# Kernel tuning notes

Measured on AMD Instinct MI355X. Metric: run time of the kernel, lower is better.

Reference implementation:

```python
import jax, jax.numpy as jnp
import numpy as np

T, B, F, H, N = 256, 256, 128, 1024, 2


def setup_inputs() -> dict:
    key = jax.random.key(0)
    ks = jax.random.split(key, 12)
    s_in = 1.0 / np.sqrt(H)  # PyTorch LSTM/Linear init scale ~ U(-1/sqrt(H), 1/sqrt(H))
    u = lambda k, shape: jax.random.uniform(k, shape, jnp.float32, -s_in, s_in)
    inp = {
        "x": jax.random.normal(ks[0], (T, B, F), jnp.float32),
        "W_ih0": u(ks[1], (4 * H, F)),
        "W_hh0": u(ks[2], (4 * H, H)),
        "b_ih0": u(ks[3], (4 * H,)),
        "b_hh0": u(ks[4], (4 * H,)),
        "W_ih1": u(ks[5], (4 * H, H)),
        "W_hh1": u(ks[6], (4 * H, H)),
        "b_ih1": u(ks[7], (4 * H,)),
        "b_hh1": u(ks[8], (4 * H,)),
        "W_lin": u(ks[9], (F, H)),
        "b_lin": u(ks[10], (F,)),
        "bs": B,
    }
    return inp


def _lstm_layer(x, W_ih, W_hh, b_ih, b_hh):
    # x: (T, B, in), returns out (T, B, H), (h_T, c_T) each (B, H)
    # Precompute input projections for all timesteps in one big GEMM.
    xW = jnp.einsum('tbf,gf->tbg', x, W_ih) + b_ih + b_hh  # (T, B, 4H)
    h0 = jnp.zeros((x.shape[1], W_hh.shape[1]), x.dtype)

    def step(carry, xw_t):
        h, c = carry
        gates = xw_t + h @ W_hh.T  # (B, 4H); PyTorch gate order i, f, g, o
        i, f, g, o = jnp.split(gates, 4, axis=-1)
        c = jax.nn.sigmoid(f) * c + jax.nn.sigmoid(i) * jnp.tanh(g)
        h = jax.nn.sigmoid(o) * jnp.tanh(c)
        return (h, c), h

    (h_T, c_T), out = jax.lax.scan(step, (h0, h0), xW)
    return out, h_T, c_T


def reference(x, W_ih0, W_hh0, b_ih0, b_hh0, W_ih1, W_hh1, b_ih1, b_hh1, W_lin, b_lin, bs):
    # Stacked 2-layer LSTM with zero initial state (self.h is None on fresh call).
    out0, h0_T, c0_T = _lstm_layer(x, W_ih0, W_hh0, b_ih0, b_hh0)
    out1, h1_T, c1_T = _lstm_layer(out0, W_ih1, W_hh1, b_ih1, b_hh1)
    # Original: y = linear(out[0]) -> first timestep of top layer output.
    y = out1[0] @ W_lin.T + b_lin  # (B, F)
    h_n = jnp.stack([h0_T, h1_T])  # (N, B, H)
    c_n = jnp.stack([c0_T, c1_T])  # (N, B, H)
    return y, h_n, c_n
```

## Files before the change

### kernel.cpp

```cpp
#include <hip/hip_runtime.h>
#include <stdint.h>


typedef __bf16 bf16x8 __attribute__((ext_vector_type(8)));
typedef float  f32x4  __attribute__((ext_vector_type(4)));
typedef unsigned short ushort8v __attribute__((ext_vector_type(8)));
typedef unsigned short ushort4v __attribute__((ext_vector_type(4)));
typedef unsigned short ushort2v __attribute__((ext_vector_type(2)));
typedef __attribute__((address_space(1))) unsigned int as1_u32;
typedef __attribute__((address_space(3))) unsigned int as3_u32;

#define T_STEPS 256
#define BATCH   256
#define HDIM    1024
#define GDIM    4096
#define FDIM    128
#define HXSLOT  (BATCH * HDIM)

static __device__ __forceinline__ float bf2f(unsigned short u) {
  union { unsigned int i; float f; } v; v.i = ((unsigned int)u) << 16; return v.f;
}
static __device__ __forceinline__ unsigned short f2bf(float f) {
  return __builtin_bit_cast(unsigned short, (__bf16)f);
}
static __device__ __forceinline__ float sigm(float x) { return 1.f / (1.f + __expf(-x)); }
static __device__ __forceinline__ float tanh_f(float x) { return 2.f / (1.f + __expf(-2.f * x)) - 1.f; }

static __device__ __forceinline__ int swz(int b) {
  return b ^ (((b >> 7) & 3) << 4);
}
static __device__ __forceinline__ int gswz(int b) {
  return b ^ (((b >> 7) & 7) << 4);
}

static __device__ __forceinline__ void vl1_inv() {
  asm volatile("buffer_inv" ::: "memory");
}

__global__ void conv_bf16(const float* __restrict__ s, unsigned short* __restrict__ d, int n) {
  int i = blockIdx.x * 256 + threadIdx.x;
  if (i < n) d[i] = f2bf(s[i]);
}

__global__ void diag_kernel(float* out, int n, float v) {
  int i = blockIdx.x * 256 + threadIdx.x;
  if (i < n) out[i] = v;
}

__device__ __forceinline__ void post_stamp(unsigned int* st, unsigned int gen, bool fast) {
  if (!fast) __builtin_amdgcn_fence(__ATOMIC_RELEASE, "agent");
  __hip_atomic_store(st, gen, __ATOMIC_RELAXED, __HIP_MEMORY_SCOPE_AGENT);
}

__device__ __forceinline__ void poll_all(unsigned int* stamps, unsigned int target) {
  unsigned int* p = stamps + (threadIdx.x & 31) * 32;
  for (unsigned int it = 0; it < (1u << 15); ++it) {
    unsigned int gv = __hip_atomic_load(p, __ATOMIC_RELAXED, __HIP_MEMORY_SCOPE_AGENT);
    if (__all((int)(gv - target) >= 0)) return;
    if (it > 16) __builtin_amdgcn_s_sleep(1);
  }
}

__device__ __forceinline__ void poll_mine(unsigned int* stamps, int g, int kh, unsigned int target) {
  unsigned int* p = stamps + (kh * 16 + g + 4 * ((int)threadIdx.x & 3)) * 32;
  for (unsigned int it = 0; it < (1u << 15); ++it) {
    unsigned int gv = __hip_atomic_load(p, __ATOMIC_RELAXED, __HIP_MEMORY_SCOPE_AGENT);
    if (__all((int)(gv - target) >= 0)) return;
    if (it > 64) __builtin_amdgcn_s_sleep(1);
  }
}

__device__ __forceinline__ void lds_spin(unsigned int* f, unsigned int need) {
  for (unsigned int it = 0; it < (1u << 15); ++it) {
    unsigned int v = __hip_atomic_load(f, __ATOMIC_ACQUIRE, __HIP_MEMORY_SCOPE_WORKGROUP);
    if ((int)(v - need) >= 0) return;
    if (it > 32) __builtin_amdgcn_s_sleep(1);
  }
}

__device__ __forceinline__ void stage_chunks(const unsigned short* __restrict__ hsrc,
                                             unsigned short* AsPtr, int r0, int g, int kh, int lane) {
  #pragma unroll
  for (int q = 0; q < 4; ++q) {
    int c = kh * 16 + g + 4 * q;
    const char* src = (const char*)(hsrc + (size_t)c * 8192 + r0 * 32);
    char* dst = (char*)AsPtr + c * 2048;
    __builtin_amdgcn_global_load_lds((const as1_u32*)(src + lane * 16), (as3_u32*)dst, 16, 0, 0);
    __builtin_amdgcn_global_load_lds((const as1_u32*)(src + 1024 + lane * 16), (as3_u32*)(dst + 1024), 16, 0, 0);
  }
}

__global__ __launch_bounds__(512, 2) void gemm_bt_xw(
    const unsigned short* __restrict__ A,
    const unsigned short* __restrict__ B,
    unsigned short* __restrict__ xw)
{
  const int tid = threadIdx.x, lane = tid & 63, wv = tid >> 6;
  const int wm = wv & 1, wn = wv >> 1;
  const int quad = lane >> 4, l15 = lane & 15;
  const int m0 = blockIdx.x * 256;
  const int n0 = blockIdx.y * 256;

  __shared__ unsigned short Ab[2][16384];
  __shared__ unsigned short Bb[2][16384];

  f32x4 acc[8][4];
  #pragma unroll
  for (int i = 0; i < 8; ++i)
    #pragma unroll
    for (int j = 0; j < 4; ++j) acc[i][j] = f32x4{0.f, 0.f, 0.f, 0.f};

  #define G2L(dst8k, src, row_org, blk_row0, kt_)                                   \
    {                                                                               \
      int o_ = wv * 1024 + lane * 16;                                               \
      int tp_ = gswz(o_);                                                           \
      int row_ = (blk_row0) + (tp_ >> 7);                                           \
      const char* g_ = (const char*)((src) + (size_t)((row_org) + row_) * 1024)     \
                       + (kt_) * 128 + (tp_ & 127);                                 \
      __builtin_amdgcn_global_load_lds((const as1_u32*)g_,                          \
          (as3_u32*)((char*)(dst8k) + wv * 1024), 16, 0, 0);                        \
    }

  #pragma unroll
  for (int b4 = 0; b4 < 4; ++b4) G2L(&Bb[0][b4 * 4096], B, n0, b4 * 64, 0);
  #pragma unroll
  for (int q4 = 0; q4 < 4; ++q4) G2L(&Ab[0][q4 * 4096], A, m0, q4 * 64, 0);
  __syncthreads();

  bf16x8 af[4][2], bfr[4][2];

  #pragma unroll 1
  for (int kt = 0; kt < 16; ++kt) {
    const int cur = kt & 1, nxt = cur ^ 1;
    const bool st = (kt < 15);

    if (st) { G2L(&Bb[nxt][0], B, n0, 0, kt + 1); G2L(&Bb[nxt][4096], B, n0, 64, kt + 1); }
    if (kt == 15)      asm volatile("s_waitcnt vmcnt(2)" ::: "memory");
    else if (kt > 0)   asm volatile("s_waitcnt vmcnt(4)" ::: "memory");
    __builtin_amdgcn_s_barrier();
    __builtin_amdgcn_sched_barrier(0);
    #pragma unroll
    for (int nt = 0; nt < 4; ++nt)
      #pragma unroll
      for (int kk = 0; kk < 2; ++kk) {
        int q = (wn * 64 + nt * 16 + l15) * 128 + kk * 64 + quad * 16;
        bfr[nt][kk] = *(const bf16x8*)((const char*)Bb[cur] + gswz(q));
      }
    #pragma unroll
    for (int mt = 0; mt < 4; ++mt)
      #pragma unroll
      for (int kk = 0; kk < 2; ++kk) {
        int q = (wm * 128 + mt * 16 + l15) * 128 + kk * 64 + quad * 16;
        af[mt][kk] = *(const bf16x8*)((const char*)Ab[cur] + gswz(q));
      }
    __builtin_amdgcn_s_setprio(1);
    #pragma unroll
    for (int mt = 0; mt < 4; ++mt)
      #pragma unroll
      for (int nt = 0; nt < 2; ++nt)
        #pragma unroll
        for (int kk = 0; kk < 2; ++kk)
          acc[mt][nt] = __builtin_amdgcn_mfma_f32_16x16x32_bf16(af[mt][kk], bfr[nt][kk], acc[mt][nt], 0, 0, 0);
    __builtin_amdgcn_s_setprio(0);
    __builtin_amdgcn_s_barrier();

    if (st) { G2L(&Bb[nxt][8192], B, n0, 128, kt + 1); G2L(&Bb[nxt][12288], B, n0, 192, kt + 1); }
    __builtin_amdgcn_s_barrier();
    __builtin_amdgcn_s_setprio(1);
    #pragma unroll
    for (int mt = 0; mt < 4; ++mt)
      #pragma unroll
      for (int nt = 0; nt < 2; ++nt)
        #pragma unroll
        for (int kk = 0; kk < 2; ++kk)
          acc[mt][nt + 2] = __builtin_amdgcn_mfma_f32_16x16x32_bf16(af[mt][kk], bfr[nt + 2][kk], acc[mt][nt + 2], 0, 0, 0);
    __builtin_amdgcn_s_setprio(0);
    __builtin_amdgcn_s_barrier();

    if (st) { G2L(&Ab[nxt][0], A, m0, 0, kt + 1); G2L(&Ab[nxt][8192], A, m0, 128, kt + 1); }
    if (kt == 15) asm volatile("s_waitcnt vmcnt(0)" ::: "memory");
    else          asm volatile("s_waitcnt vmcnt(6)" ::: "memory");
    __builtin_amdgcn_s_barrier();
    __builtin_amdgcn_sched_barrier(0);
    #pragma unroll
    for (int mt = 0; mt < 4; ++mt)
      #pragma unroll
      for (int kk = 0; kk < 2; ++kk) {
        int q = (wm * 128 + 64 + mt * 16 + l15) * 128 + kk * 64 + quad * 16;
        af[mt][kk] = *(const bf16x8*)((const char*)Ab[cur] + gswz(q));
      }
    __builtin_amdgcn_s_setprio(1);
    #pragma unroll
    for (int mt = 0; mt < 4; ++mt)
      #pragma unroll
      for (int nt = 0; nt < 2; ++nt)
        #pragma unroll
        for (int kk = 0; kk < 2; ++kk)
          acc[mt + 4][nt] = __builtin_amdgcn_mfma_f32_16x16x32_bf16(af[mt][kk], bfr[nt][kk], acc[mt + 4][nt], 0, 0, 0);
    __builtin_amdgcn_s_setprio(0);
    __builtin_amdgcn_s_barrier();

    if (st) { G2L(&Ab[nxt][4096], A, m0, 64, kt + 1); G2L(&Ab[nxt][12288], A, m0, 192, kt + 1); }
    __builtin_amdgcn_s_barrier();
    __builtin_amdgcn_s_setprio(1);
    #pragma unroll
    for (int mt = 0; mt < 4; ++mt)
      #pragma unroll
      for (int nt = 0; nt < 2; ++nt)
        #pragma unroll
        for (int kk = 0; kk < 2; ++kk)
          acc[mt + 4][nt + 2] = __builtin_amdgcn_mfma_f32_16x16x32_bf16(af[mt][kk], bfr[nt + 2][kk], acc[mt + 4][nt + 2], 0, 0, 0);
    __builtin_amdgcn_s_setprio(0);
    __builtin_amdgcn_s_barrier();
  }
  #undef G2L

  #pragma unroll
  for (int mt = 0; mt < 8; ++mt) {
    int ml = wm * 128 + mt * 16 + quad * 4;
    #pragma unroll
    for (int nt = 0; nt < 4; ++nt) {
      int col = n0 + wn * 64 + nt * 16 + l15;
      ushort4v v;
      v.x = f2bf(acc[mt][nt][0]); v.y = f2bf(acc[mt][nt][1]);
      v.z = f2bf(acc[mt][nt][2]); v.w = f2bf(acc[mt][nt][3]);
      *(ushort4v*)(xw + ((size_t)blockIdx.x * GDIM + col) * BATCH + ml) = v;
    }
  }
}

__device__ __forceinline__ bool probe_chk(unsigned int* probeBuf, unsigned int* stamps,
                                          unsigned int salt, unsigned int target,
                                          unsigned int* flagLds) {
  const int wg = blockIdx.x, mi = wg & 7, ni = wg >> 3;
  const int tid = threadIdx.x;
  if (tid == 0) probeBuf[wg * 32] = salt ^ (unsigned int)wg;
  __syncthreads();
  if (tid == 0)
    __hip_atomic_store(stamps + ni * 32, target, __ATOMIC_RELAXED, __HIP_MEMORY_SCOPE_AGENT);
  poll_all(stamps, target);
  vl1_inv();
  if (tid == 0) {
    unsigned int bad = 0;
    for (int k = 0; k < 32; ++k) {
      int member = mi + 8 * k;
      unsigned int v = probeBuf[member * 32];
      if (v != (salt ^ (unsigned int)member)) bad = 1;
    }
    *flagLds = bad;
  }
  __syncthreads();
  return (*flagLds == 0);
}

__global__ __launch_bounds__(512, 2) void lstm_layer0_kernel(
    const unsigned short* __restrict__ xbf,
    const float* __restrict__ Wih,
    const float* __restrict__ Whh,
    const float* __restrict__ bih,
    const float* __restrict__ bhh,
    unsigned short* __restrict__ slab,
    unsigned short* __restrict__ hx,
    float* __restrict__ cstate,
    int t0, int ch_len, unsigned int gen_base,
    float* __restrict__ dout_h,
    float* __restrict__ dout_c,
    unsigned int* __restrict__ bar,
    unsigned int* __restrict__ probe)
{
  const int tid = threadIdx.x, lane = tid & 63, wv = tid >> 6;
  const int quad = lane >> 4, l15 = lane & 15;
  const int g = wv & 3, kh = wv >> 2;
  const int wg = blockIdx.x;
  const int mi = wg & 7, ni = wg >> 3;
  const int r0 = mi * 32, hc0 = ni * 32;
  unsigned int* stamps = bar + mi * 1024;

  __shared__ unsigned short As[32 * 1024];
  __shared__ float gbuf[8][32][33];
  __shared__ unsigned int cflag[8];
  __shared__ unsigned int flagLds;

  if (tid < 8) cflag[tid] = 0;

  bf16x8 whh[2][16];
  #pragma unroll
  for (int nt = 0; nt < 2; ++nt) {
    #pragma unroll
    for (int sl = 0; sl < 16; ++sl) {
      int jj = ((g + (sl >> 2)) & 3) + 4 * (sl & 3);
      const float* wrow = Whh + (size_t)(g * HDIM + hc0 + nt * 16 + l15) * HDIM + kh * 512 + jj * 32 + quad * 8;
      f32x4 f0 = *(const f32x4*)(wrow);
      f32x4 f1 = *(const f32x4*)(wrow + 4);
      bf16x8 r;
      r[0] = (__bf16)f0[0]; r[1] = (__bf16)f0[1]; r[2] = (__bf16)f0[2]; r[3] = (__bf16)f0[3];
      r[4] = (__bf16)f1[0]; r[5] = (__bf16)f1[1]; r[6] = (__bf16)f1[2]; r[7] = (__bf16)f1[3];
      whh[nt][sl] = r;
    }
  }
  bf16x8 wih[2][2];
  #pragma unroll
  for (int nt = 0; nt < 2; ++nt) {
    const float* wrow = Wih + (size_t)(g * HDIM + hc0 + nt * 16 + l15) * FDIM + kh * 64 + quad * 8;
    #pragma unroll
    for (int kk = 0; kk < 2; ++kk) {
      f32x4 f0 = *(const f32x4*)(wrow + kk * 32);
      f32x4 f1 = *(const f32x4*)(wrow + kk * 32 + 4);
      bf16x8 r;
      r[0] = (__bf16)f0[0]; r[1] = (__bf16)f0[1]; r[2] = (__bf16)f0[2]; r[3] = (__bf16)f0[3];
      r[4] = (__bf16)f1[0]; r[5] = (__bf16)f1[1]; r[6] = (__bf16)f1[2]; r[7] = (__bf16)f1[3];
      wih[nt][kk] = r;
    }
  }

  const int hcl = tid & 31, rg2 = tid >> 5;
  float bias[4];
  #pragma unroll
  for (int b4 = 0; b4 < 4; ++b4)
    bias[b4] = bih[b4 * HDIM + hc0 + hcl] + bhh[b4 * HDIM + hc0 + hcl];

  float c[2];
  #pragma unroll
  for (int r = 0; r < 2; ++r)
    c[r] = (t0 == 0) ? 0.f : cstate[(size_t)(r0 + rg2 * 2 + r) * HDIM + hc0 + hcl];

  unsigned int salt = 0x9E3779B9u ^ (gen_base * 2654435761u);
  bool fast = probe_chk(probe, stamps, salt, gen_base + 1u, &flagLds);

  const int tend = t0 + ch_len;

  if (t0 > 0) {
    stage_chunks(hx + (size_t)((t0 - 1) & 1) * HXSLOT, As, r0, g, kh, lane);
    asm volatile("s_waitcnt vmcnt(0)" ::: "memory");
    if (lane == 0)
      __hip_atomic_store(&cflag[kh * 4 + g], gen_base + 1u, __ATOMIC_RELEASE, __HIP_MEMORY_SCOPE_WORKGROUP);
  }

  f32x4 acc[2][2];
  #pragma unroll
  for (int mt = 0; mt < 2; ++mt)
    #pragma unroll
    for (int nt = 0; nt < 2; ++nt) acc[mt][nt] = f32x4{0.f, 0.f, 0.f, 0.f};
  #pragma unroll
  for (int j = 0; j < 2; ++j) {
    bf16x8 af[2];
    #pragma unroll
    for (int mt = 0; mt < 2; ++mt)
      af[mt] = *(const bf16x8*)(xbf + (size_t)(t0 * BATCH + r0 + mt * 16 + l15) * FDIM + kh * 64 + j * 32 + quad * 8);
    #pragma unroll
    for (int mt = 0; mt < 2; ++mt)
      #pragma unroll
      for (int nt = 0; nt < 2; ++nt)
        acc[mt][nt] = __builtin_amdgcn_mfma_f32_16x16x32_bf16(af[mt], wih[nt][j], acc[mt][nt], 0, 0, 0);
  }

  #pragma unroll 1
  for (int t = t0; t < tend; ++t) {
    if (t > 0) {
      const unsigned int need = gen_base + 1u + (unsigned int)(t - t0);
      #pragma unroll
      for (int sl = 0; sl < 16; ++sl) {
        const int s = sl >> 2, q = sl & 3;
        int sg = (g + s) & 3;
        if (q == 0 && s > 0) lds_spin(&cflag[kh * 4 + sg], need);
        int cidx = kh * 16 + sg + 4 * q;
        bf16x8 af[2];
        #pragma unroll
        for (int mt = 0; mt < 2; ++mt) {
          int bo = (mt * 16 + l15) * 64 + quad * 16;
          bo = swz(bo);
          af[mt] = *(const bf16x8*)((const char*)As + cidx * 2048 + bo);
        }
        #pragma unroll
        for (int mt = 0; mt < 2; ++mt)
          #pragma unroll
          for (int nt = 0; nt < 2; ++nt)
            acc[mt][nt] = __builtin_amdgcn_mfma_f32_16x16x32_bf16(af[mt], whh[nt][sl], acc[mt][nt], 0, 0, 0);
      }
    }

    #pragma unroll
    for (int mt = 0; mt < 2; ++mt)
      #pragma unroll
      for (int nt = 0; nt < 2; ++nt) {
        int hl = nt * 16 + l15;
        int rq = mt * 16 + quad * 4;
        #pragma unroll
        for (int i = 0; i < 4; ++i)
          gbuf[wv][hl][rq + i] = acc[mt][nt][i];
      }
    __syncthreads();

    unsigned short* hdst = slab + (size_t)(t - t0 + 1) * (BATCH * HDIM);
    unsigned short* hxd  = hx + (size_t)(t & 1) * HXSLOT;
    #pragma unroll
    for (int r = 0; r < 2; ++r) {
      int row = rg2 * 2 + r;
      float gi = gbuf[0][hcl][row] + gbuf[4][hcl][row] + bias[0];
      float gf = gbuf[1][hcl][row] + gbuf[5][hcl][row] + bias[1];
      float gg = gbuf[2][hcl][row] + gbuf[6][hcl][row] + bias[2];
      float go = gbuf[3][hcl][row] + gbuf[7][hcl][row] + bias[3];
      float iv = sigm(gi), fv = sigm(gf), gv = tanh_f(gg), ov = sigm(go);
      float cn = fv * c[r] + iv * gv;
      c[r] = cn;
      float hv = ov * tanh_f(cn);
      unsigned short hb = f2bf(hv);
      int boff = swz(row * 64 + hcl * 2);
      hxd[ni * 8192 + mi * 1024 + (boff >> 1)] = hb;
      int gidx = (r0 + row) * HDIM + hc0 + hcl;
      hdst[gidx] = hb;
      if (t == tend - 1) cstate[gidx] = cn;
      if (t == T_STEPS - 1) { dout_h[gidx] = hv; dout_c[gidx] = cn; }
    }
    __syncthreads();

    if (t != tend - 1) {
      const unsigned int tgt = gen_base + 2u + (unsigned int)(t - t0);
      if (tid == 0) post_stamp(stamps + ni * 32, tgt, fast);

      #pragma unroll
      for (int mt = 0; mt < 2; ++mt)
        #pragma unroll
        for (int nt = 0; nt < 2; ++nt) acc[mt][nt] = f32x4{0.f, 0.f, 0.f, 0.f};
      #pragma unroll
      for (int j = 0; j < 2; ++j) {
        bf16x8 af[2];
        #pragma unroll
        for (int mt = 0; mt < 2; ++mt)
          af[mt] = *(const bf16x8*)(xbf + (size_t)((t + 1) * BATCH + r0 + mt * 16 + l15) * FDIM + kh * 64 + j * 32 + quad * 8);
        #pragma unroll
        for (int mt = 0; mt < 2; ++mt)
          #pragma unroll
          for (int nt = 0; nt < 2; ++nt)
            acc[mt][nt] = __builtin_amdgcn_mfma_f32_16x16x32_bf16(af[mt], wih[nt][j], acc[mt][nt], 0, 0, 0);
      }

      poll_mine(stamps, g, kh, tgt);
      if (fast) vl1_inv();
      else __builtin_amdgcn_fence(__ATOMIC_ACQUIRE, "agent");
      stage_chunks(hx + (size_t)(t & 1) * HXSLOT, As, r0, g, kh, lane);
      asm volatile("s_waitcnt vmcnt(0)" ::: "memory");
      if (lane == 0)
        __hip_atomic_store(&cflag[kh * 4 + g], tgt, __ATOMIC_RELEASE, __HIP_MEMORY_SCOPE_WORKGROUP);
    }
  }
}

__global__ __launch_bounds__(512, 2) void lstm_layer1_kernel(
    const unsigned short* __restrict__ xw,
    const float* __restrict__ Whh,
    const float* __restrict__ bih,
    const float* __restrict__ bhh,
    unsigned short* __restrict__ hpp,
    float* __restrict__ cstate,
    int t0, int ch_len, unsigned int gen_base,
    unsigned short* __restrict__ h1t0,
    float* __restrict__ dout_h,
    float* __restrict__ dout_c,
    unsigned int* __restrict__ bar,
    unsigned int* __restrict__ probe)
{
  const int tid = threadIdx.x, lane = tid & 63, wv = tid >> 6;
  const int quad = lane >> 4, l15 = lane & 15;
  const int g = wv & 3, kh = wv >> 2;
  const int wg = blockIdx.x;
  const int mi = wg & 7, ni = wg >> 3;
  const int r0 = mi * 32, hc0 = ni * 32;
  unsigned int* stamps = bar + mi * 1024;

  __shared__ unsigned short As[32 * 1024];
  __shared__ float gbuf[8][32][33];
  __shared__ unsigned int cflag[8];
  __shared__ unsigned int flagLds;

  if (tid < 8) cflag[tid] = 0;

  bf16x8 whh[2][16];
  #pragma unroll
  for (int nt = 0; nt < 2; ++nt) {
    #pragma unroll
    for (int sl = 0; sl < 16; ++sl) {
      int jj = ((g + (sl >> 2)) & 3) + 4 * (sl & 3);
      const float* wrow = Whh + (size_t)(g * HDIM + hc0 + nt * 16 + l15) * HDIM + kh * 512 + jj * 32 + quad * 8;
      f32x4 f0 = *(const f32x4*)(wrow);
      f32x4 f1 = *(const f32x4*)(wrow + 4);
      bf16x8 r;
      r[0] = (__bf16)f0[0]; r[1] = (__bf16)f0[1]; r[2] = (__bf16)f0[2]; r[3] = (__bf16)f0[3];
      r[4] = (__bf16)f1[0]; r[5] = (__bf16)f1[1]; r[6] = (__bf16)f1[2]; r[7] = (__bf16)f1[3];
      whh[nt][sl] = r;
    }
  }

  const int hcl = tid & 31, rg2 = tid >> 5;
  float bias[4];
  #pragma unroll
  for (int b4 = 0; b4 < 4; ++b4)
    bias[b4] = bih[b4 * HDIM + hc0 + hcl] + bhh[b4 * HDIM + hc0 + hcl];

  float c[2];
  #pragma unroll
  for (int r = 0; r < 2; ++r)
    c[r] = (t0 == 0) ? 0.f : cstate[(size_t)(r0 + rg2 * 2 + r) * HDIM + hc0 + hcl];

  unsigned int salt = 0xB5297A4Du ^ (gen_base * 2654435761u);
  bool fast = probe_chk(probe, stamps, salt, gen_base + 1u, &flagLds);

  const int tend = t0 + ch_len;

  if (t0 > 0) {
    stage_chunks(hpp + (size_t)((t0 - 1) & 1) * HXSLOT, As, r0, g, kh, lane);
    asm volatile("s_waitcnt vmcnt(0)" ::: "memory");
    if (lane == 0)
      __hip_atomic_store(&cflag[kh * 4 + g], gen_base + 1u, __ATOMIC_RELEASE, __HIP_MEMORY_SCOPE_WORKGROUP);
  }

  float xwv[4][2];
  #pragma unroll
  for (int g4 = 0; g4 < 4; ++g4) {
    const unsigned short* xp =
        xw + ((size_t)0 * GDIM + g4 * HDIM + hc0 + hcl) * BATCH + r0 + rg2 * 2;
    ushort2v u = *(const ushort2v*)xp;
    xwv[g4][0] = bf2f(u.x); xwv[g4][1] = bf2f(u.y);
  }

  #pragma unroll 1
  for (int t = t0; t < tend; ++t) {
    f32x4 acc[2][2];
    #pragma unroll
    for (int mt = 0; mt < 2; ++mt)
      #pragma unroll
      for (int nt = 0; nt < 2; ++nt) acc[mt][nt] = f32x4{0.f, 0.f, 0.f, 0.f};

    if (t > 0) {
      const unsigned int need = gen_base + 1u + (unsigned int)(t - t0);
      #pragma unroll
      for (int sl = 0; sl < 16; ++sl) {
        const int s = sl >> 2, q = sl & 3;
        int sg = (g + s) & 3;
        if (q == 0 && s > 0) lds_spin(&cflag[kh * 4 + sg], need);
        int cidx = kh * 16 + sg + 4 * q;
        bf16x8 af[2];
        #pragma unroll
        for (int mt = 0; mt < 2; ++mt) {
          int bo = (mt * 16 + l15) * 64 + quad * 16;
          bo = swz(bo);
          af[mt] = *(const bf16x8*)((const char*)As + cidx * 2048 + bo);
        }
        #pragma unroll
        for (int mt = 0; mt < 2; ++mt)
          #pragma unroll
          for (int nt = 0; nt < 2; ++nt)
            acc[mt][nt] = __builtin_amdgcn_mfma_f32_16x16x32_bf16(af[mt], whh[nt][sl], acc[mt][nt], 0, 0, 0);
      }
    }

    #pragma unroll
    for (int mt = 0; mt < 2; ++mt)
      #pragma unroll
      for (int nt = 0; nt < 2; ++nt) {
        int hl = nt * 16 + l15;
        int rq = mt * 16 + quad * 4;
        #pragma unroll
        for (int i = 0; i < 4; ++i)
          gbuf[wv][hl][rq + i] = acc[mt][nt][i];
      }
    __syncthreads();

    unsigned short* hxd = hpp + (size_t)(t & 1) * HXSLOT;
    #pragma unroll
    for (int r = 0; r < 2; ++r) {
      int row = rg2 * 2 + r;
      float gi = gbuf[0][hcl][row] + gbuf[4][hcl][row] + xwv[0][r] + bias[0];
      float gf = gbuf[1][hcl][row] + gbuf[5][hcl][row] + xwv[1][r] + bias[1];
      float gg = gbuf[2][hcl][row] + gbuf[6][hcl][row] + xwv[2][r] + bias[2];
      float go = gbuf[3][hcl][row] + gbuf[7][hcl][row] + xwv[3][r] + bias[3];
      float iv = sigm(gi), fv = sigm(gf), gv = tanh_f(gg), ov = sigm(go);
      float cn = fv * c[r] + iv * gv;
      c[r] = cn;
      float hv = ov * tanh_f(cn);
      unsigned short hb = f2bf(hv);
      int boff = swz(row * 64 + hcl * 2);
      hxd[ni * 8192 + mi * 1024 + (boff >> 1)] = hb;
      int gidx = (r0 + row) * HDIM + hc0 + hcl;
      if (h1t0 != nullptr && t == 0) h1t0[gidx] = hb;
      if (t == tend - 1) cstate[gidx] = cn;
      if (t == T_STEPS - 1) { dout_h[gidx] = hv; dout_c[gidx] = cn; }
    }
    __syncthreads();

    if (t != tend - 1) {
      const unsigned int tgt = gen_base + 2u + (unsigned int)(t - t0);
      if (tid == 0) post_stamp(stamps + ni * 32, tgt, fast);

      #pragma unroll
      for (int g4 = 0; g4 < 4; ++g4) {
        const unsigned short* xp =
            xw + ((size_t)(t + 1 - t0) * GDIM + g4 * HDIM + hc0 + hcl) * BATCH + r0 + rg2 * 2;
        ushort2v u = *(const ushort2v*)xp;
        xwv[g4][0] = bf2f(u.x); xwv[g4][1] = bf2f(u.y);
      }

      poll_mine(stamps, g, kh, tgt);
      if (fast) vl1_inv();
      else __builtin_amdgcn_fence(__ATOMIC_ACQUIRE, "agent");
      stage_chunks(hpp + (size_t)(t & 1) * HXSLOT, As, r0, g, kh, lane);
      asm volatile("s_waitcnt vmcnt(0)" ::: "memory");
      if (lane == 0)
        __hip_atomic_store(&cflag[kh * 4 + g], tgt, __ATOMIC_RELEASE, __HIP_MEMORY_SCOPE_WORKGROUP);
    }
  }
}

__global__ void y_kernel(const unsigned short* __restrict__ h1t0,
                         const unsigned short* __restrict__ wlin,
                         const float* __restrict__ blin,
                         float* __restrict__ y)
{
  int b = blockIdx.x;
  int f = threadIdx.x;
  const ushort8v* hp = (const ushort8v*)(h1t0 + (size_t)b * HDIM);
  const ushort8v* wp = (const ushort8v*)(wlin + (size_t)f * HDIM);
  float acc = 0.f;
  for (int i = 0; i < HDIM / 8; ++i) {
    ushort8v hv = hp[i], wvv = wp[i];
    #pragma unroll
    for (int j = 0; j < 8; ++j) acc += bf2f(hv[j]) * bf2f(wvv[j]);
  }
  y[b * FDIM + f] = acc + blin[f];
}

extern "C" void kernel_launch(void* const* d_in, const int* in_sizes, int n_in,
                              void* d_out, int out_size, void* d_ws, size_t ws_size,
                              hipStream_t stream) {
  (void)in_sizes; (void)n_in; (void)out_size;
  const float* x    = (const float*)d_in[0];
  const float* Wih0 = (const float*)d_in[1];
  const float* Whh0 = (const float*)d_in[2];
  const float* bih0 = (const float*)d_in[3];
  const float* bhh0 = (const float*)d_in[4];
  const float* Wih1 = (const float*)d_in[5];
  const float* Whh1 = (const float*)d_in[6];
  const float* bih1 = (const float*)d_in[7];
  const float* bhh1 = (const float*)d_in[8];
  const float* Wlin = (const float*)d_in[9];
  const float* blin = (const float*)d_in[10];
  float* out = (float*)d_out;

  const size_t SZ_BAR   = 32768;
  const size_t SZ_PROBE = 32768;
  const size_t SZ_XBF   = (size_t)T_STEPS * BATCH * FDIM * 2;
  const size_t SZ_WIH1  = (size_t)GDIM * HDIM * 2;
  const size_t SZ_WLIN  = (size_t)FDIM * HDIM * 2;
  const size_t SZ_HPP   = (size_t)2 * BATCH * HDIM * 2;
  const size_t SZ_HX    = (size_t)2 * BATCH * HDIM * 2;
  const size_t SZ_H1T0  = (size_t)BATCH * HDIM * 2;
  const size_t SZ_CST   = (size_t)BATCH * HDIM * 4;
  const size_t SLOT     = (size_t)BATCH * HDIM * 2;
  const size_t fixed = SZ_BAR + SZ_PROBE + SZ_XBF + SZ_WIH1 + SZ_WLIN + SZ_HPP + SZ_HX + SZ_H1T0 + 2 * SZ_CST;

  int CH = 0;
  const int cands[7] = {256, 128, 64, 32, 16, 8, 4};
  for (int i = 0; i < 7; ++i) {
    int c = cands[i];
    size_t need = fixed + (size_t)(c + 1) * SLOT + (size_t)c * GDIM * BATCH * 2;
    if (need <= ws_size) { CH = c; break; }
  }
  if (CH == 0) {
    float v = 1.0e6f + (float)(ws_size >> 20);
    diag_kernel<<<(32768 + 255) / 256, 256, 0, stream>>>(out, 32768, v);
    return;
  }

  char* ws = (char*)d_ws;
  size_t o = 0;
  unsigned int*   bar   = (unsigned int*)(ws + o);    o += SZ_BAR;
  unsigned int*   probe = (unsigned int*)(ws + o);    o += SZ_PROBE;
  unsigned short* xbf   = (unsigned short*)(ws + o);  o += SZ_XBF;
  unsigned short* wih1b = (unsigned short*)(ws + o);  o += SZ_WIH1;
  unsigned short* wlinb = (unsigned short*)(ws + o);  o += SZ_WLIN;
  unsigned short* h1pp  = (unsigned short*)(ws + o);  o += SZ_HPP;
  unsigned short* hx0   = (unsigned short*)(ws + o);  o += SZ_HX;
  unsigned short* h1t0  = (unsigned short*)(ws + o);  o += SZ_H1T0;
  float*          c0st  = (float*)(ws + o);           o += SZ_CST;
  float*          c1st  = (float*)(ws + o);           o += SZ_CST;
  unsigned short* slab  = (unsigned short*)(ws + o);  o += (size_t)(CH + 1) * SLOT;
  unsigned short* xw1   = (unsigned short*)(ws + o);  o += (size_t)CH * GDIM * BATCH * 2;

  hipMemsetAsync(bar, 0, SZ_BAR, stream);

  conv_bf16<<<(T_STEPS * BATCH * FDIM + 255) / 256, 256, 0, stream>>>(x, xbf, T_STEPS * BATCH * FDIM);
  conv_bf16<<<(GDIM * HDIM + 255) / 256, 256, 0, stream>>>(Wih1, wih1b, GDIM * HDIM);
  conv_bf16<<<(FDIM * HDIM + 255) / 256, 256, 0, stream>>>(Wlin, wlinb, FDIM * HDIM);

  float* hn0 = out + 32768;
  float* hn1 = out + 32768 + 262144;
  float* cn0 = out + 32768 + 524288;
  float* cn1 = out + 32768 + 524288 + 262144;

  unsigned int gen_base = 0;
  for (int ch = 0; ch < T_STEPS / CH; ++ch) {
    int t0 = ch * CH;
    lstm_layer0_kernel<<<256, 512, 0, stream>>>(
        xbf, Wih0, Whh0, bih0, bhh0, slab, hx0, c0st, t0, CH, gen_base, hn0, cn0, bar, probe);
    gen_base += (unsigned int)CH;
    gemm_bt_xw<<<dim3(CH, 16), 512, 0, stream>>>(
        slab + BATCH * HDIM, wih1b, xw1);
    lstm_layer1_kernel<<<256, 512, 0, stream>>>(
        xw1, Whh1, bih1, bhh1, h1pp, c1st, t0, CH, gen_base, h1t0, hn1, cn1, bar, probe);
    gen_base += (unsigned int)CH;
  }

  y_kernel<<<256, 128, 0, stream>>>(h1t0, wlinb, blin, out);
}
```

Baseline: 3.291 ms.

## Fuse both LSTM layers into one launch, pipelining layer1 one chunk behind layer0

Merges the two recurrent layer kernels into one templated body and launches a single 512-block kernel. The first 256 blocks run layer 0 on chunk ch while the other 256 run layer 1 on chunk ch-1, so the two recurrences overlap instead of running one after the other. To fit two blocks per CU, the LDS staging buffer for h is halved: each timestep loads and consumes the hidden state in two row halves, with a workgroup counter gating the reuse of the buffer. Chunk length is capped at 128 so the pipeline has more than one stage. This relies on all 512 blocks being resident at once for the spin barriers, and it adds intra-step LDS synchronisation.

```diff
diff --git a/kernel.cpp b/kernel.cpp
--- a/kernel.cpp
+++ b/kernel.cpp
@@ -15,7 +15,7 @@
 #define HDIM    1024
 #define GDIM    4096
 #define FDIM    128
-#define HXSLOT  (BATCH * HDIM)
+#define HXSLOTB (524288)
 
 static __device__ __forceinline__ float bf2f(unsigned short u) {
   union { unsigned int i; float f; } v; v.i = ((unsigned int)u) << 16; return v.f;
@@ -26,7 +26,7 @@
 static __device__ __forceinline__ float sigm(float x) { return 1.f / (1.f + __expf(-x)); }
 static __device__ __forceinline__ float tanh_f(float x) { return 2.f / (1.f + __expf(-2.f * x)) - 1.f; }
 
-static __device__ __forceinline__ int swz(int b) {
+static __device__ __forceinline__ int swz1(int b) {
   return b ^ (((b >> 7) & 3) << 4);
 }
 static __device__ __forceinline__ int gswz(int b) {
@@ -78,15 +78,21 @@
   }
 }
 
-__device__ __forceinline__ void stage_chunks(const unsigned short* __restrict__ hsrc,
-                                             unsigned short* AsPtr, int r0, int g, int kh, int lane) {
+__device__ __forceinline__ void rdone_spin(unsigned int* f, unsigned int need) {
+  for (unsigned int it = 0; it < (1u << 15); ++it) {
+    unsigned int v = __hip_atomic_load(f, __ATOMIC_RELAXED, __HIP_MEMORY_SCOPE_WORKGROUP);
+    if ((int)(v - need) >= 0) return;
+  }
+}
+
+__device__ __forceinline__ void stage_pump(const char* hslotB, unsigned short* AsPtr,
+                                           int mi, int g, int kh, int p, int lane) {
   #pragma unroll
   for (int q = 0; q < 4; ++q) {
     int c = kh * 16 + g + 4 * q;
-    const char* src = (const char*)(hsrc + (size_t)c * 8192 + r0 * 32);
-    char* dst = (char*)AsPtr + c * 2048;
-    __builtin_amdgcn_global_load_lds((const as1_u32*)(src + lane * 16), (as3_u32*)dst, 16, 0, 0);
-    __builtin_amdgcn_global_load_lds((const as1_u32*)(src + 1024 + lane * 16), (as3_u32*)(dst + 1024), 16, 0, 0);
+    const char* src = hslotB + (size_t)c * 16384 + mi * 2048 + p * 1024 + lane * 16;
+    char* dst = (char*)AsPtr + c * 1024;
+    __builtin_amdgcn_global_load_lds((const as1_u32*)src, (as3_u32*)dst, 16, 0, 0);
   }
 }
 
@@ -231,10 +237,9 @@
 
 __device__ __forceinline__ bool probe_chk(unsigned int* probeBuf, unsigned int* stamps,
                                           unsigned int salt, unsigned int target,
-                                          unsigned int* flagLds) {
-  const int wg = blockIdx.x, mi = wg & 7, ni = wg >> 3;
+                                          unsigned int* flagLds, int tokIdx, int tokBase, int mi, int ni) {
   const int tid = threadIdx.x;
-  if (tid == 0) probeBuf[wg * 32] = salt ^ (unsigned int)wg;
+  if (tid == 0) probeBuf[tokIdx * 32] = salt ^ (unsigned int)tokIdx;
   __syncthreads();
   if (tid == 0)
     __hip_atomic_store(stamps + ni * 32, target, __ATOMIC_RELAXED, __HIP_MEMORY_SCOPE_AGENT);
@@ -243,7 +248,7 @@
   if (tid == 0) {
     unsigned int bad = 0;
     for (int k = 0; k < 32; ++k) {
-      int member = mi + 8 * k;
+      int member = tokBase + mi + 8 * k;
       unsigned int v = probeBuf[member * 32];
       if (v != (salt ^ (unsigned int)member)) bad = 1;
     }
@@ -253,35 +258,31 @@
   return (*flagLds == 0);
 }
 
-__global__ __launch_bounds__(512, 2) void lstm_layer0_kernel(
-    const unsigned short* __restrict__ xbf,
+template<bool L1>
+__device__ __forceinline__ void lstm_body(
+    const unsigned short* __restrict__ xin,
     const float* __restrict__ Wih,
     const float* __restrict__ Whh,
     const float* __restrict__ bih,
     const float* __restrict__ bhh,
     unsigned short* __restrict__ slab,
-    unsigned short* __restrict__ hx,
+    unsigned short* __restrict__ hexch,
     float* __restrict__ cstate,
-    int t0, int ch_len, unsigned int gen_base,
+    unsigned short* __restrict__ h1t0,
     float* __restrict__ dout_h,
     float* __restrict__ dout_c,
-    unsigned int* __restrict__ bar,
-    unsigned int* __restrict__ probe)
+    int t0, int ch_len, unsigned int gen_base,
+    unsigned int* __restrict__ stamps,
+    unsigned int* __restrict__ probeBuf, int tokIdx, int tokBase,
+    int mi, int ni,
+    unsigned short* As, float (*gbuf)[32][33],
+    unsigned int (*cflag)[8], unsigned int* rdone, unsigned int* flagLds)
 {
   const int tid = threadIdx.x, lane = tid & 63, wv = tid >> 6;
   const int quad = lane >> 4, l15 = lane & 15;
   const int g = wv & 3, kh = wv >> 2;
-  const int wg = blockIdx.x;
-  const int mi = wg & 7, ni = wg >> 3;
   const int r0 = mi * 32, hc0 = ni * 32;
-  unsigned int* stamps = bar + mi * 1024;
-
-  __shared__ unsigned short As[32 * 1024];
-  __shared__ float gbuf[8][32][33];
-  __shared__ unsigned int cflag[8];
-  __shared__ unsigned int flagLds;
-
-  if (tid < 8) cflag[tid] = 0;
+  const int aoff = swz1(l15 * 64 + quad * 16);
 
   bf16x8 whh[2][16];
   #pragma unroll
@@ -299,17 +300,19 @@
     }
   }
   bf16x8 wih[2][2];
-  #pragma unroll
-  for (int nt = 0; nt < 2; ++nt) {
-    const float* wrow = Wih + (size_t)(g * HDIM + hc0 + nt * 16 + l15) * FDIM + kh * 64 + quad * 8;
-    #pragma unroll
-    for (int kk = 0; kk < 2; ++kk) {
-      f32x4 f0 = *(const f32x4*)(wrow + kk * 32);
-      f32x4 f1 = *(const f32x4*)(wrow + kk * 32 + 4);
-      bf16x8 r;
-      r[0] = (__bf16)f0[0]; r[1] = (__bf16)f0[1]; r[2] = (__bf16)f0[2]; r[3] = (__bf16)f0[3];
-      r[4] = (__bf16)f1[0]; r[5] = (__bf16)f1[1]; r[6] = (__bf16)f1[2]; r[7] = (__bf16)f1[3];
-      wih[nt][kk] = r;
+  if constexpr (!L1) {
+    #pragma unroll
+    for (int nt = 0; nt < 2; ++nt) {
+      const float* wrow = Wih + (size_t)(g * HDIM + hc0 + nt * 16 + l15) * FDIM + kh * 64 + quad * 8;
+      #pragma unroll
+      for (int kk = 0; kk < 2; ++kk) {
+        f32x4 f0 = *(const f32x4*)(wrow + kk * 32);
+        f32x4 f1 = *(const f32x4*)(wrow + kk * 32 + 4);
+        bf16x8 r;
+        r[0] = (__bf16)f0[0]; r[1] = (__bf16)f0[1]; r[2] = (__bf16)f0[2]; r[3] = (__bf16)f0[3];
+        r[4] = (__bf16)f1[0]; r[5] = (__bf16)f1[1]; r[6] = (__bf16)f1[2]; r[7] = (__bf16)f1[3];
+        wih[nt][kk] = r;
+      }
     }
   }
 
@@ -324,16 +327,16 @@
   for (int r = 0; r < 2; ++r)
     c[r] = (t0 == 0) ? 0.f : cstate[(size_t)(r0 + rg2 * 2 + r) * HDIM + hc0 + hcl];
 
-  unsigned int salt = 0x9E3779B9u ^ (gen_base * 2654435761u);
-  bool fast = probe_chk(probe, stamps, salt, gen_base + 1u, &flagLds);
+  unsigned int salt = (L1 ? 0xB5297A4Du : 0x9E3779B9u) ^ (gen_base * 2654435761u);
+  bool fast = probe_chk(probeBuf, stamps, salt, gen_base + 1u, flagLds, tokIdx, tokBase, mi, ni);
 
   const int tend = t0 + ch_len;
 
   if (t0 > 0) {
-    stage_chunks(hx + (size_t)((t0 - 1) & 1) * HXSLOT, As, r0, g, kh, lane);
+    stage_pump((const char*)hexch + (size_t)((t0 - 1) & 1) * HXSLOTB, As, mi, g, kh, 0, lane);
     asm volatile("s_waitcnt vmcnt(0)" ::: "memory");
     if (lane == 0)
-      __hip_atomic_store(&cflag[kh * 4 + g], gen_base + 1u, __ATOMIC_RELEASE, __HIP_MEMORY_SCOPE_WORKGROUP);
+      __hip_atomic_store(&cflag[0][kh * 4 + g], gen_base + 1u, __ATOMIC_RELEASE, __HIP_MEMORY_SCOPE_WORKGROUP);
   }
 
   f32x4 acc[2][2];
@@ -341,18 +344,30 @@
   for (int mt = 0; mt < 2; ++mt)
     #pragma unroll
     for (int nt = 0; nt < 2; ++nt) acc[mt][nt] = f32x4{0.f, 0.f, 0.f, 0.f};
-  #pragma unroll
-  for (int j = 0; j < 2; ++j) {
-    bf16x8 af[2];
-    #pragma unroll
-    for (int mt = 0; mt < 2; ++mt)
-      af[mt] = *(const bf16x8*)(xbf + (size_t)(t0 * BATCH + r0 + mt * 16 + l15) * FDIM + kh * 64 + j * 32 + quad * 8);
-    #pragma unroll
-    for (int mt = 0; mt < 2; ++mt)
-      #pragma unroll
-      for (int nt = 0; nt < 2; ++nt)
-        acc[mt][nt] = __builtin_amdgcn_mfma_f32_16x16x32_bf16(af[mt], wih[nt][j], acc[mt][nt], 0, 0, 0);
-  }
+  float xwv[4][2];
+  if constexpr (!L1) {
+    #pragma unroll
+    for (int j = 0; j < 2; ++j) {
+      bf16x8 af[2];
+      #pragma unroll
+      for (int mt = 0; mt < 2; ++mt)
+        af[mt] = *(const bf16x8*)(xin + (size_t)(t0 * BATCH + r0 + mt * 16 + l15) * FDIM + kh * 64 + j * 32 + quad * 8);
+      #pragma unroll
+      for (int mt = 0; mt < 2; ++mt)
+        #pragma unroll
+        for (int nt = 0; nt < 2; ++nt)
+          acc[mt][nt] = __builtin_amdgcn_mfma_f32_16x16x32_bf16(af[mt], wih[nt][j], acc[mt][nt], 0, 0, 0);
+    }
+  } else {
+    #pragma unroll
+    for (int g4 = 0; g4 < 4; ++g4) {
+      const unsigned short* xp = xin + ((size_t)0 * GDIM + g4 * HDIM + hc0 + hcl) * BATCH + r0 + rg2 * 2;
+      ushort2v u = *(const ushort2v*)xp;
+      xwv[g4][0] = bf2f(u.x); xwv[g4][1] = bf2f(u.y);
+    }
+  }
+
+  unsigned int pumptgt = 0;
 
   #pragma unroll 1
   for (int t = t0; t < tend; ++t) {
@@ -362,37 +377,52 @@
       for (int sl = 0; sl < 16; ++sl) {
         const int s = sl >> 2, q = sl & 3;
         int sg = (g + s) & 3;
-        if (q == 0 && s > 0) lds_spin(&cflag[kh * 4 + sg], need);
+        if (q == 0 && s > 0) lds_spin(&cflag[0][kh * 4 + sg], need);
         int cidx = kh * 16 + sg + 4 * q;
-        bf16x8 af[2];
-        #pragma unroll
-        for (int mt = 0; mt < 2; ++mt) {
-          int bo = (mt * 16 + l15) * 64 + quad * 16;
-          bo = swz(bo);
-          af[mt] = *(const bf16x8*)((const char*)As + cidx * 2048 + bo);
-        }
-        #pragma unroll
-        for (int mt = 0; mt < 2; ++mt)
-          #pragma unroll
-          for (int nt = 0; nt < 2; ++nt)
-            acc[mt][nt] = __builtin_amdgcn_mfma_f32_16x16x32_bf16(af[mt], whh[nt][sl], acc[mt][nt], 0, 0, 0);
-      }
-    }
-
-    #pragma unroll
-    for (int mt = 0; mt < 2; ++mt)
-      #pragma unroll
-      for (int nt = 0; nt < 2; ++nt) {
-        int hl = nt * 16 + l15;
-        int rq = mt * 16 + quad * 4;
+        bf16x8 af = *(const bf16x8*)((const char*)As + cidx * 1024 + aoff);
+        acc[0][0] = __builtin_amdgcn_mfma_f32_16x16x32_bf16(af, whh[0][sl], acc[0][0], 0, 0, 0);
+        acc[0][1] = __builtin_amdgcn_mfma_f32_16x16x32_bf16(af, whh[1][sl], acc[0][1], 0, 0, 0);
+      }
+      #pragma unroll
+      for (int nt = 0; nt < 2; ++nt)
         #pragma unroll
         for (int i = 0; i < 4; ++i)
-          gbuf[wv][hl][rq + i] = acc[mt][nt][i];
-      }
+          gbuf[wv][nt * 16 + l15][quad * 4 + i] = acc[0][nt][i];
+      if (lane == 0)
+        __hip_atomic_fetch_add(&rdone[kh], 1u, __ATOMIC_RELAXED, __HIP_MEMORY_SCOPE_WORKGROUP);
+      pumptgt += 4;
+      rdone_spin(&rdone[kh], pumptgt);
+      stage_pump((const char*)hexch + (size_t)((t - 1) & 1) * HXSLOTB, As, mi, g, kh, 1, lane);
+      asm volatile("s_waitcnt vmcnt(0)" ::: "memory");
+      if (lane == 0)
+        __hip_atomic_store(&cflag[1][kh * 4 + g], need, __ATOMIC_RELEASE, __HIP_MEMORY_SCOPE_WORKGROUP);
+      #pragma unroll
+      for (int sl = 0; sl < 16; ++sl) {
+        const int s = sl >> 2, q = sl & 3;
+        int sg = (g + s) & 3;
+        if (q == 0 && s > 0) lds_spin(&cflag[1][kh * 4 + sg], need);
+        int cidx = kh * 16 + sg + 4 * q;
+        bf16x8 af = *(const bf16x8*)((const char*)As + cidx * 1024 + aoff);
+        acc[1][0] = __builtin_amdgcn_mfma_f32_16x16x32_bf16(af, whh[0][sl], acc[1][0], 0, 0, 0);
+        acc[1][1] = __builtin_amdgcn_mfma_f32_16x16x32_bf16(af, whh[1][sl], acc[1][1], 0, 0, 0);
+      }
+    } else {
+      #pragma unroll
+      for (int nt = 0; nt < 2; ++nt)
+        #pragma unroll
+        for (int i = 0; i < 4; ++i)
+          gbuf[wv][nt * 16 + l15][quad * 4 + i] = acc[0][nt][i];
+    }
+    #pragma unroll
+    for (int nt = 0; nt < 2; ++nt)
+      #pragma unroll
+      for (int i = 0; i < 4; ++i)
+        gbuf[wv][nt * 16 + l15][16 + quad * 4 + i] = acc[1][nt][i];
     __syncthreads();
 
-    unsigned short* hdst = slab + (size_t)(t - t0 + 1) * (BATCH * HDIM);
-    unsigned short* hxd  = hx + (size_t)(t & 1) * HXSLOT;
+    char* hxdB = (char*)hexch + (size_t)(t & 1) * HXSLOTB;
+    unsigned short* hdst = nullptr;
+    if constexpr (!L1) hdst = slab + (size_t)(t - t0 + 1) * (BATCH * HDIM);
     #pragma unroll
     for (int r = 0; r < 2; ++r) {
       int row = rg2 * 2 + r;
@@ -400,15 +430,19 @@
       float gf = gbuf[1][hcl][row] + gbuf[5][hcl][row] + bias[1];
       float gg = gbuf[2][hcl][row] + gbuf[6][hcl][row] + bias[2];
       float go = gbuf[3][hcl][row] + gbuf[7][hcl][row] + bias[3];
+      if constexpr (L1) {
+        gi += xwv[0][r]; gf += xwv[1][r]; gg += xwv[2][r]; go += xwv[3][r];
+      }
       float iv = sigm(gi), fv = sigm(gf), gv = tanh_f(gg), ov = sigm(go);
       float cn = fv * c[r] + iv * gv;
       c[r] = cn;
       float hv = ov * tanh_f(cn);
       unsigned short hb = f2bf(hv);
-      int boff = swz(row * 64 + hcl * 2);
-      hxd[ni * 8192 + mi * 1024 + (boff >> 1)] = hb;
+      int boff = swz1((row & 15) * 64 + hcl * 2);
+      *(unsigned short*)(hxdB + (size_t)ni * 16384 + mi * 2048 + (row >> 4) * 1024 + boff) = hb;
       int gidx = (r0 + row) * HDIM + hc0 + hcl;
-      hdst[gidx] = hb;
+      if constexpr (!L1) hdst[gidx] = hb;
+      if constexpr (L1) { if (h1t0 != nullptr && t == 0) h1t0[gidx] = hb; }
       if (t == tend - 1) cstate[gidx] = cn;
       if (t == T_STEPS - 1) { dout_h[gidx] = hv; dout_c[gidx] = cn; }
     }
@@ -422,192 +456,80 @@
       for (int mt = 0; mt < 2; ++mt)
         #pragma unroll
         for (int nt = 0; nt < 2; ++nt) acc[mt][nt] = f32x4{0.f, 0.f, 0.f, 0.f};
-      #pragma unroll
-      for (int j = 0; j < 2; ++j) {
-        bf16x8 af[2];
-        #pragma unroll
-        for (int mt = 0; mt < 2; ++mt)
-          af[mt] = *(const bf16x8*)(xbf + (size_t)((t + 1) * BATCH + r0 + mt * 16 + l15) * FDIM + kh * 64 + j * 32 + quad * 8);
-        #pragma unroll
-        for (int mt = 0; mt < 2; ++mt)
+      if constexpr (!L1) {
+        #pragma unroll
+        for (int j = 0; j < 2; ++j) {
+          bf16x8 af[2];
           #pragma unroll
-          for (int nt = 0; nt < 2; ++nt)
-            acc[mt][nt] = __builtin_amdgcn_mfma_f32_16x16x32_bf16(af[mt], wih[nt][j], acc[mt][nt], 0, 0, 0);
+          for (int mt = 0; mt < 2; ++mt)
+            af[mt] = *(const bf16x8*)(xin + (size_t)((t + 1) * BATCH + r0 + mt * 16 + l15) * FDIM + kh * 64 + j * 32 + quad * 8);
+          #pragma unroll
+          for (int mt = 0; mt < 2; ++mt)
+            #pragma unroll
+            for (int nt = 0; nt < 2; ++nt)
+              acc[mt][nt] = __builtin_amdgcn_mfma_f32_16x16x32_bf16(af[mt], wih[nt][j], acc[mt][nt], 0, 0, 0);
+        }
+      } else {
+        #pragma unroll
+        for (int g4 = 0; g4 < 4; ++g4) {
+          const unsigned short* xp = xin + ((size_t)(t + 1 - t0) * GDIM + g4 * HDIM + hc0 + hcl) * BATCH + r0 + rg2 * 2;
+          ushort2v u = *(const ushort2v*)xp;
+          xwv[g4][0] = bf2f(u.x); xwv[g4][1] = bf2f(u.y);
+        }
       }
 
       poll_mine(stamps, g, kh, tgt);
       if (fast) vl1_inv();
       else __builtin_amdgcn_fence(__ATOMIC_ACQUIRE, "agent");
-      stage_chunks(hx + (size_t)(t & 1) * HXSLOT, As, r0, g, kh, lane);
+      stage_pump((const char*)hexch + (size_t)(t & 1) * HXSLOTB, As, mi, g, kh, 0, lane);
       asm volatile("s_waitcnt vmcnt(0)" ::: "memory");
       if (lane == 0)
-        __hip_atomic_store(&cflag[kh * 4 + g], tgt, __ATOMIC_RELEASE, __HIP_MEMORY_SCOPE_WORKGROUP);
-    }
-  }
-}
-
-__global__ __launch_bounds__(512, 2) void lstm_layer1_kernel(
-    const unsigned short* __restrict__ xw,
-    const float* __restrict__ Whh,
-    const float* __restrict__ bih,
-    const float* __restrict__ bhh,
-    unsigned short* __restrict__ hpp,
-    float* __restrict__ cstate,
-    int t0, int ch_len, unsigned int gen_base,
+        __hip_atomic_store(&cflag[0][kh * 4 + g], tgt, __ATOMIC_RELEASE, __HIP_MEMORY_SCOPE_WORKGROUP);
+    }
+  }
+}
+
+__global__ __launch_bounds__(512, 2) void lstm_fused(
+    const unsigned short* __restrict__ xbf,
+    const float* __restrict__ Wih0, const float* __restrict__ Whh0,
+    const float* __restrict__ bih0, const float* __restrict__ bhh0,
+    unsigned short* __restrict__ slab, unsigned short* __restrict__ hx,
+    float* __restrict__ c0st,
+    const unsigned short* __restrict__ xw, const float* __restrict__ Whh1,
+    const float* __restrict__ bih1, const float* __restrict__ bhh1,
+    unsigned short* __restrict__ hpp, float* __restrict__ c1st,
     unsigned short* __restrict__ h1t0,
-    float* __restrict__ dout_h,
-    float* __restrict__ dout_c,
-    unsigned int* __restrict__ bar,
-    unsigned int* __restrict__ probe)
+    float* __restrict__ hn0, float* __restrict__ cn0,
+    float* __restrict__ hn1, float* __restrict__ cn1,
+    unsigned int* __restrict__ bar, unsigned int* __restrict__ probe,
+    int t0_0, int t0_1, int ch_len, unsigned int gen0, unsigned int gen1)
 {
-  const int tid = threadIdx.x, lane = tid & 63, wv = tid >> 6;
-  const int quad = lane >> 4, l15 = lane & 15;
-  const int g = wv & 3, kh = wv >> 2;
-  const int wg = blockIdx.x;
-  const int mi = wg & 7, ni = wg >> 3;
-  const int r0 = mi * 32, hc0 = ni * 32;
-  unsigned int* stamps = bar + mi * 1024;
-
-  __shared__ unsigned short As[32 * 1024];
+  __shared__ unsigned short As[32 * 512];
   __shared__ float gbuf[8][32][33];
-  __shared__ unsigned int cflag[8];
+  __shared__ unsigned int cflag[2][8];
+  __shared__ unsigned int rdone[4];
   __shared__ unsigned int flagLds;
 
-  if (tid < 8) cflag[tid] = 0;
-
-  bf16x8 whh[2][16];
-  #pragma unroll
-  for (int nt = 0; nt < 2; ++nt) {
-    #pragma unroll
-    for (int sl = 0; sl < 16; ++sl) {
-      int jj = ((g + (sl >> 2)) & 3) + 4 * (sl & 3);
-      const float* wrow = Whh + (size_t)(g * HDIM + hc0 + nt * 16 + l15) * HDIM + kh * 512 + jj * 32 + quad * 8;
-      f32x4 f0 = *(const f32x4*)(wrow);
-      f32x4 f1 = *(const f32x4*)(wrow + 4);
-      bf16x8 r;
-      r[0] = (__bf16)f0[0]; r[1] = (__bf16)f0[1]; r[2] = (__bf16)f0[2]; r[3] = (__bf16)f0[3];
-      r[4] = (__bf16)f1[0]; r[5] = (__bf16)f1[1]; r[6] = (__bf16)f1[2]; r[7] = (__bf16)f1[3];
-      whh[nt][sl] = r;
-    }
-  }
-
-  const int hcl = tid & 31, rg2 = tid >> 5;
-  float bias[4];
-  #pragma unroll
-  for (int b4 = 0; b4 < 4; ++b4)
-    bias[b4] = bih[b4 * HDIM + hc0 + hcl] + bhh[b4 * HDIM + hc0 + hcl];
-
-  float c[2];
-  #pragma unroll
-  for (int r = 0; r < 2; ++r)
-    c[r] = (t0 == 0) ? 0.f : cstate[(size_t)(r0 + rg2 * 2 + r) * HDIM + hc0 + hcl];
-
-  unsigned int salt = 0xB5297A4Du ^ (gen_base * 2654435761u);
-  bool fast = probe_chk(probe, stamps, salt, gen_base + 1u, &flagLds);
-
-  const int tend = t0 + ch_len;
-
-  if (t0 > 0) {
-    stage_chunks(hpp + (size_t)((t0 - 1) & 1) * HXSLOT, As, r0, g, kh, lane);
-    asm volatile("s_waitcnt vmcnt(0)" ::: "memory");
-    if (lane == 0)
-      __hip_atomic_store(&cflag[kh * 4 + g], gen_base + 1u, __ATOMIC_RELEASE, __HIP_MEMORY_SCOPE_WORKGROUP);
-  }
-
-  float xwv[4][2];
-  #pragma unroll
-  for (int g4 = 0; g4 < 4; ++g4) {
-    const unsigned short* xp =
-        xw + ((size_t)0 * GDIM + g4 * HDIM + hc0 + hcl) * BATCH + r0 + rg2 * 2;
-    ushort2v u = *(const ushort2v*)xp;
-    xwv[g4][0] = bf2f(u.x); xwv[g4][1] = bf2f(u.y);
-  }
-
-  #pragma unroll 1
-  for (int t = t0; t < tend; ++t) {
-    f32x4 acc[2][2];
-    #pragma unroll
-    for (int mt = 0; mt < 2; ++mt)
-      #pragma unroll
-      for (int nt = 0; nt < 2; ++nt) acc[mt][nt] = f32x4{0.f, 0.f, 0.f, 0.f};
-
-    if (t > 0) {
-      const unsigned int need = gen_base + 1u + (unsigned int)(t - t0);
-      #pragma unroll
-      for (int sl = 0; sl < 16; ++sl) {
-        const int s = sl >> 2, q = sl & 3;
-        int sg = (g + s) & 3;
-        if (q == 0 && s > 0) lds_spin(&cflag[kh * 4 + sg], need);
-        int cidx = kh * 16 + sg + 4 * q;
-        bf16x8 af[2];
-        #pragma unroll
-        for (int mt = 0; mt < 2; ++mt) {
-          int bo = (mt * 16 + l15) * 64 + quad * 16;
-          bo = swz(bo);
-          af[mt] = *(const bf16x8*)((const char*)As + cidx * 2048 + bo);
-        }
-        #pragma unroll
-        for (int mt = 0; mt < 2; ++mt)
-          #pragma unroll
-          for (int nt = 0; nt < 2; ++nt)
-            acc[mt][nt] = __builtin_amdgcn_mfma_f32_16x16x32_bf16(af[mt], whh[nt][sl], acc[mt][nt], 0, 0, 0);
-      }
-    }
-
-    #pragma unroll
-    for (int mt = 0; mt < 2; ++mt)
-      #pragma unroll
-      for (int nt = 0; nt < 2; ++nt) {
-        int hl = nt * 16 + l15;
-        int rq = mt * 16 + quad * 4;
-        #pragma unroll
-        for (int i = 0; i < 4; ++i)
-          gbuf[wv][hl][rq + i] = acc[mt][nt][i];
-      }
-    __syncthreads();
-
-    unsigned short* hxd = hpp + (size_t)(t & 1) * HXSLOT;
-    #pragma unroll
-    for (int r = 0; r < 2; ++r) {
-      int row = rg2 * 2 + r;
-      float gi = gbuf[0][hcl][row] + gbuf[4][hcl][row] + xwv[0][r] + bias[0];
-      float gf = gbuf[1][hcl][row] + gbuf[5][hcl][row] + xwv[1][r] + bias[1];
-      float gg = gbuf[2][hcl][row] + gbuf[6][hcl][row] + xwv[2][r] + bias[2];
-      float go = gbuf[3][hcl][row] + gbuf[7][hcl][row] + xwv[3][r] + bias[3];
-      float iv = sigm(gi), fv = sigm(gf), gv = tanh_f(gg), ov = sigm(go);
-      float cn = fv * c[r] + iv * gv;
-      c[r] = cn;
-      float hv = ov * tanh_f(cn);
-      unsigned short hb = f2bf(hv);
-      int boff = swz(row * 64 + hcl * 2);
-      hxd[ni * 8192 + mi * 1024 + (boff >> 1)] = hb;
-      int gidx = (r0 + row) * HDIM + hc0 + hcl;
-      if (h1t0 != nullptr && t == 0) h1t0[gidx] = hb;
-      if (t == tend - 1) cstate[gidx] = cn;
-      if (t == T_STEPS - 1) { dout_h[gidx] = hv; dout_c[gidx] = cn; }
-    }
-    __syncthreads();
-
-    if (t != tend - 1) {
-      const unsigned int tgt = gen_base + 2u + (unsigned int)(t - t0);
-      if (tid == 0) post_stamp(stamps + ni * 32, tgt, fast);
-
-      #pragma unroll
-      for (int g4 = 0; g4 < 4; ++g4) {
-        const unsigned short* xp =
-            xw + ((size_t)(t + 1 - t0) * GDIM + g4 * HDIM + hc0 + hcl) * BATCH + r0 + rg2 * 2;
-        ushort2v u = *(const ushort2v*)xp;
-        xwv[g4][0] = bf2f(u.x); xwv[g4][1] = bf2f(u.y);
-      }
-
-      poll_mine(stamps, g, kh, tgt);
-      if (fast) vl1_inv();
-      else __builtin_amdgcn_fence(__ATOMIC_ACQUIRE, "agent");
-      stage_chunks(hpp + (size_t)(t & 1) * HXSLOT, As, r0, g, kh, lane);
-      asm volatile("s_waitcnt vmcnt(0)" ::: "memory");
-      if (lane == 0)
-        __hip_atomic_store(&cflag[kh * 4 + g], tgt, __ATOMIC_RELEASE, __HIP_MEMORY_SCOPE_WORKGROUP);
-    }
+  const int tid = threadIdx.x;
+  if (tid < 16) ((unsigned int*)cflag)[tid] = 0;
+  if (tid < 4) rdone[tid] = 0;
+
+  const int bx = blockIdx.x;
+  if (bx < 256) {
+    if (t0_0 < 0) return;
+    const int mi = bx & 7, ni = bx >> 3;
+    lstm_body<false>(xbf, Wih0, Whh0, bih0, bhh0, slab, hx, c0st, nullptr,
+                     hn0, cn0, t0_0, ch_len, gen0,
+                     bar + mi * 1024, probe, bx, 0, mi, ni,
+                     As, gbuf, cflag, rdone, &flagLds);
+  } else {
+    if (t0_1 < 0) return;
+    const int wg = bx - 256;
+    const int mi = wg & 7, ni = wg >> 3;
+    lstm_body<true>(xw, nullptr, Whh1, bih1, bhh1, nullptr, hpp, c1st, h1t0,
+                    hn1, cn1, t0_1, ch_len, gen1,
+                    bar + (8 + mi) * 1024, probe, bx, 256, mi, ni,
+                    As, gbuf, cflag, rdone, &flagLds);
   }
 }
 
@@ -646,8 +568,8 @@
   const float* blin = (const float*)d_in[10];
   float* out = (float*)d_out;
 
-  const size_t SZ_BAR   = 32768;
-  const size_t SZ_PROBE = 32768;
+  const size_t SZ_BAR   = 65536;
+  const size_t SZ_PROBE = 65536;
   const size_t SZ_XBF   = (size_t)T_STEPS * BATCH * FDIM * 2;
   const size_t SZ_WIH1  = (size_t)GDIM * HDIM * 2;
   const size_t SZ_WLIN  = (size_t)FDIM * HDIM * 2;
@@ -665,6 +587,7 @@
     size_t need = fixed + (size_t)(c + 1) * SLOT + (size_t)c * GDIM * BATCH * 2;
     if (need <= ws_size) { CH = c; break; }
   }
+  if (CH == 0 || CH == 256) CH = (CH == 256) ? 128 : 0;
   if (CH == 0) {
     float v = 1.0e6f + (float)(ws_size >> 20);
     diag_kernel<<<(32768 + 255) / 256, 256, 0, stream>>>(out, 32768, v);
@@ -697,17 +620,19 @@
   float* cn0 = out + 32768 + 524288;
   float* cn1 = out + 32768 + 524288 + 262144;
 
-  unsigned int gen_base = 0;
-  for (int ch = 0; ch < T_STEPS / CH; ++ch) {
-    int t0 = ch * CH;
-    lstm_layer0_kernel<<<256, 512, 0, stream>>>(
-        xbf, Wih0, Whh0, bih0, bhh0, slab, hx0, c0st, t0, CH, gen_base, hn0, cn0, bar, probe);
-    gen_base += (unsigned int)CH;
-    gemm_bt_xw<<<dim3(CH, 16), 512, 0, stream>>>(
-        slab + BATCH * HDIM, wih1b, xw1);
-    lstm_layer1_kernel<<<256, 512, 0, stream>>>(
-        xw1, Whh1, bih1, bhh1, h1pp, c1st, t0, CH, gen_base, h1t0, hn1, cn1, bar, probe);
-    gen_base += (unsigned int)CH;
+  const int NCH = T_STEPS / CH;
+  for (int ch = 0; ch <= NCH; ++ch) {
+    int t0_0 = (ch < NCH) ? ch * CH : -1;
+    int t0_1 = (ch >= 1) ? (ch - 1) * CH : -1;
+    unsigned int gen0 = (unsigned int)(ch * CH);
+    unsigned int gen1 = (ch >= 1) ? (unsigned int)((ch - 1) * CH) : 0u;
+    lstm_fused<<<512, 512, 0, stream>>>(
+        xbf, Wih0, Whh0, bih0, bhh0, slab, hx0, c0st,
+        xw1, Whh1, bih1, bhh1, h1pp, c1st, h1t0,
+        hn0, cn0, hn1, cn1, bar, probe,
+        t0_0, t0_1, CH, gen0, gen1);
+    if (ch < NCH)
+      gemm_bt_xw<<<dim3(CH, 16), 512, 0, stream>>>(slab + BATCH * HDIM, wih1b, xw1);
   }
 
   y_kernel<<<256, 128, 0, stream>>>(h1t0, wlinb, blin, out);
```

Result: slower. 3.565 ms (+8.3%).
